# Kernel optimization log

Measured on AMD Instinct MI355X. Metric: run time of the kernel, lower is better.

Reference implementation:

```python
import jax, jax.numpy as jnp
import numpy as np
from jax import lax

EPS = 1e-7
N_CLASS = 10
ROUTINGS = 3
DIM_PRIMARY = 8
DIM_DIGIT = 16


def squash(s, axis=-1):
    sq = jnp.sum(jnp.square(s), axis=axis, keepdims=True)
    scale = sq / (1.0 + sq) / jnp.sqrt(sq + EPS)
    return scale * s


def setup_inputs() -> dict:
    key = jax.random.key(0)
    ks = jax.random.split(key, 6)
    B, H, W, C = 16, 100, 64, 1
    x = jax.random.normal(ks[0], (B, H, W, C), dtype=jnp.float32)
    # conv1: 9x9, 1 -> 256, stride 1, valid, relu
    conv1_w = jax.random.normal(ks[1], (9, 9, 1, 256), dtype=jnp.float32) * 0.05
    conv1_b = jnp.zeros((256,), dtype=jnp.float32)
    # PrimaryCap conv: 9x9, 256 -> 32*8=256, stride 2, valid, linear
    pc_w = jax.random.normal(ks[2], (9, 9, 256, 256), dtype=jnp.float32) * 0.02
    pc_b = jnp.zeros((256,), dtype=jnp.float32)
    # primary caps: conv1 out 92x56 -> pc conv out 42x24 -> 42*24*32 = 32256 caps
    n_in_caps = 42 * 24 * 32
    caps_W = jax.random.normal(ks[3], (N_CLASS, n_in_caps, DIM_DIGIT, DIM_PRIMARY), dtype=jnp.float32) * 0.05
    return {"x": x, "conv1_w": conv1_w, "conv1_b": conv1_b, "pc_w": pc_w, "pc_b": pc_b, "caps_W": caps_W}


def reference(x, conv1_w, conv1_b, pc_w, pc_b, caps_W):
    dn = ("NHWC", "HWIO", "NHWC")
    # Conv1 + relu: [B,92,56,256]
    y = lax.conv_general_dilated(x, conv1_w, (1, 1), "VALID", dimension_numbers=dn) + conv1_b
    y = jax.nn.relu(y)
    # PrimaryCap conv (stride 2): [B,42,24,256]
    p = lax.conv_general_dilated(y, pc_w, (2, 2), "VALID", dimension_numbers=dn) + pc_b
    B = p.shape[0]
    # reshape to capsules [B, I, 8] and squash
    u = squash(p.reshape(B, -1, DIM_PRIMARY))
    # predictions u_hat[b,j,i,d] = W[j,i,d,k] u[b,i,k]  -> [B, J, I, 16]
    u_hat = jnp.einsum("bik,jidk->bjid", u, caps_W)
    # dynamic routing
    b = jnp.zeros(u_hat.shape[:3], dtype=u_hat.dtype)  # [B, J, I]
    v = None
    for r in range(ROUTINGS):
        c = jax.nn.softmax(b, axis=1)  # over output capsules J
        s = jnp.einsum("bji,bjid->bjd", c, u_hat)
        v = squash(s)  # [B, J, 16]
        if r < ROUTINGS - 1:
            b = b + jnp.einsum("bjd,bjid->bji", v, u_hat)
    return v
```

## Files before the change

### kernel.cpp

```cpp
#include <hip/hip_runtime.h>
#include <hip/hip_bf16.h>
#include <hip/hip_fp16.h>
#include <stdint.h>

typedef __bf16 bf16x8_t __attribute__((ext_vector_type(8)));
typedef float  f32x4_t  __attribute__((ext_vector_type(4)));

#define PLANE_H   (16L * 32256 * 32)
#define PSTRIDE_H 4128768L

__device__ __forceinline__ void gld_lds16(const void* g, void* l) {
    __builtin_amdgcn_global_load_lds(
        (const __attribute__((address_space(1))) uint32_t*)g,
        (__attribute__((address_space(3))) uint32_t*)l, 16, 0, 0);
}

__global__ __launch_bounds__(256) void k_conv1(
    const float* __restrict__ x, const float* __restrict__ w,
    const float* __restrict__ bias, __hip_bfloat16* __restrict__ y)
{
    const int b  = blockIdx.x / 92;
    const int oh = blockIdx.x % 92;
    const int oc = threadIdx.x;
    float wr[81];
#pragma unroll
    for (int t = 0; t < 81; ++t) wr[t] = w[t * 256 + oc];
    const float bs = bias[oc];
    const float* xb = x + (b * 100 + oh) * 64;
    __hip_bfloat16* yb = y + ((b * 92 + oh) * 56) * 256 + oc;
    for (int owg = 0; owg < 56; owg += 4) {
        float a0 = bs, a1 = bs, a2 = bs, a3 = bs;
#pragma unroll
        for (int kh = 0; kh < 9; ++kh) {
            const float* xr = xb + kh * 64 + owg;
            float xv[12];
#pragma unroll
            for (int t = 0; t < 12; ++t) xv[t] = xr[t];
#pragma unroll
            for (int kw = 0; kw < 9; ++kw) {
                const float wv = wr[kh * 9 + kw];
                a0 = fmaf(xv[kw + 0], wv, a0);
                a1 = fmaf(xv[kw + 1], wv, a1);
                a2 = fmaf(xv[kw + 2], wv, a2);
                a3 = fmaf(xv[kw + 3], wv, a3);
            }
        }
        yb[(owg + 0) * 256] = __float2bfloat16(fmaxf(a0, 0.f));
        yb[(owg + 1) * 256] = __float2bfloat16(fmaxf(a1, 0.f));
        yb[(owg + 2) * 256] = __float2bfloat16(fmaxf(a2, 0.f));
        yb[(owg + 3) * 256] = __float2bfloat16(fmaxf(a3, 0.f));
    }
}

__global__ __launch_bounds__(256) void k_wt(
    const float* __restrict__ w, __hip_bfloat16* __restrict__ wt)
{
    const int idx = blockIdx.x * 256 + threadIdx.x;
    const int oc  = idx / 20736;
    const int k   = idx - oc * 20736;
    wt[idx] = __float2bfloat16(w[k * 256 + oc]);
}

__global__ __launch_bounds__(256, 4) void k_pcconv3(
    const __hip_bfloat16* __restrict__ y,
    const __hip_bfloat16* __restrict__ wt,
    __half* __restrict__ pbase)
{
    __shared__ __hip_bfloat16 lA[128 * 64];
    __shared__ __hip_bfloat16 lB[128 * 64];
    const int gx  = blockIdx.x;
    const int nb  = gx & 1;
    const int tm  = gx >> 1;
    const int mbx = (tm & 7) * 16 + (tm >> 3);
    if (mbx >= 126) return;
    const int z = blockIdx.y;
    __half* __restrict__ p = pbase + (long)z * PSTRIDE_H;

    const int tid  = threadIdx.x;
    const int lane = tid & 63;
    const int w    = tid >> 6;
    const int oct  = lane >> 3;
    const int c    = (lane & 7) ^ oct;

    int ybaseA[4], wbB[4];
#pragma unroll
    for (int j = 0; j < 4; ++j) {
        const int r  = w * 32 + j * 8 + oct;
        const int m  = mbx * 128 + r;
        const int b  = m / 1008;
        const int rm = m - b * 1008;
        const int oh = rm / 24;
        const int ow = rm - oh * 24;
        ybaseA[j] = ((b * 92 + 2 * oh) * 56 + 2 * ow) * 256 + c * 8;
        wbB[j]    = (nb * 128 + r) * 20736 + c * 8;
    }

    f32x4_t acc[4][4];
#pragma unroll
    for (int mi = 0; mi < 4; ++mi)
#pragma unroll
        for (int ni = 0; ni < 4; ++ni)
            acc[mi][ni] = (f32x4_t){0.f, 0.f, 0.f, 0.f};

    const int mw = (w >> 1) * 64;
    const int nw = (w & 1) * 64;
    const int lr = lane & 15;
    const int lq = lane >> 4;
    const int koff0 = ((lq + 0) ^ (lr & 7)) * 8;
    const int koff1 = ((lq + 4) ^ (lr & 7)) * 8;

    const int off = (gx * 11 + z * 5) % 27;
    for (int it = 0; it < 27; ++it) {
        const int kc   = z * 27 + ((it + off) % 27);
        const int k0   = kc * 64;
        const int khw  = k0 >> 8;
        const int ic0  = k0 & 255;
        const int kh   = khw / 9;
        const int kw2  = khw - kh * 9;
        const int aoff = (kh * 56 + kw2) * 256 + ic0;
        __syncthreads();
#pragma unroll
        for (int j = 0; j < 4; ++j)
            gld_lds16(y + ybaseA[j] + aoff, &lA[(w * 32 + j * 8) * 64 + lane * 8]);
#pragma unroll
        for (int j = 0; j < 4; ++j)
            gld_lds16(wt + wbB[j] + k0, &lB[(w * 32 + j * 8) * 64 + lane * 8]);
        __builtin_amdgcn_s_waitcnt(0);
        __syncthreads();
#pragma unroll
        for (int t = 0; t < 2; ++t) {
            const int koff = t ? koff1 : koff0;
            bf16x8_t af[4], bfr[4];
#pragma unroll
            for (int mi = 0; mi < 4; ++mi)
                af[mi] = *(const bf16x8_t*)&lA[(mw + mi * 16 + lr) * 64 + koff];
#pragma unroll
            for (int ni = 0; ni < 4; ++ni)
                bfr[ni] = *(const bf16x8_t*)&lB[(nw + ni * 16 + lr) * 64 + koff];
#pragma unroll
            for (int mi = 0; mi < 4; ++mi)
#pragma unroll
                for (int ni = 0; ni < 4; ++ni)
                    acc[mi][ni] = __builtin_amdgcn_mfma_f32_16x16x32_bf16(
                        af[mi], bfr[ni], acc[mi][ni], 0, 0, 0);
        }
    }
#pragma unroll
    for (int mi = 0; mi < 4; ++mi)
#pragma unroll
        for (int ni = 0; ni < 4; ++ni) {
            const int col = nb * 128 + nw + ni * 16 + lr;
#pragma unroll
            for (int rr = 0; rr < 4; ++rr) {
                const int row = mbx * 128 + mw + mi * 16 + lq * 4 + rr;
                p[(long)row * 256 + col] = __float2half(acc[mi][ni][rr]);
            }
        }
}

__global__ __launch_bounds__(512, 2) void k_pcconv8(
    const __hip_bfloat16* __restrict__ y,
    const __hip_bfloat16* __restrict__ wt,
    __half* __restrict__ pbase)
{
    extern __shared__ __hip_bfloat16 sm[];
    __hip_bfloat16* sA = sm;
    __hip_bfloat16* sB = sm + 32768;

    const int mblk = blockIdx.x;
    const int z    = blockIdx.y;
    __half* __restrict__ p = pbase + (long)z * PSTRIDE_H;

    const int tid  = threadIdx.x;
    const int lane = tid & 63;
    const int w    = tid >> 6;
    const int wm   = w >> 2;
    const int wn   = w & 3;
    const int oct  = lane >> 3;
    const int c    = (lane & 7) ^ oct;

    int ybs[4], wbs[4];
#pragma unroll
    for (int i64 = 0; i64 < 4; ++i64) {
        const int r  = i64 * 64 + w * 8 + oct;
        const int m  = mblk * 256 + r;
        const int b  = m / 1008;
        const int rm = m - b * 1008;
        const int oh = rm / 24;
        const int ow = rm - oh * 24;
        ybs[i64] = ((b * 92 + 2 * oh) * 56 + 2 * ow) * 256 + c * 8;
        wbs[i64] = r * 20736 + c * 8;
    }
    const int kbase = z * 1728;

    auto aoffk = [&](int k0) {
        const int khw = k0 >> 8;
        const int kh  = khw / 9;
        return (kh * 56 + (khw - kh * 9)) * 256 + (k0 & 255);
    };
    auto stA = [&](int i64, int buf, int aoff) {
        gld_lds16(y + ybs[i64] + aoff, sA + buf * 16384 + (i64 * 64 + w * 8) * 64 + lane * 8);
    };
    auto stB = [&](int i64, int buf, int k0) {
        gld_lds16(wt + wbs[i64] + k0, sB + buf * 16384 + (i64 * 64 + w * 8) * 64 + lane * 8);
    };

    f32x4_t acc[2][4][2][2];
#pragma unroll
    for (int mh = 0; mh < 2; ++mh)
#pragma unroll
        for (int mi = 0; mi < 4; ++mi)
#pragma unroll
            for (int nh = 0; nh < 2; ++nh)
#pragma unroll
                for (int ni = 0; ni < 2; ++ni)
                    acc[mh][mi][nh][ni] = (f32x4_t){0.f, 0.f, 0.f, 0.f};

    const int lr = lane & 15;
    const int lq = lane >> 4;
    const int koff0 = ((lq + 0) ^ (lr & 7)) * 8;
    const int koff1 = ((lq + 4) ^ (lr & 7)) * 8;

    bf16x8_t af[4][2], bf0[2][2], bf1[2][2];

#define RD_A(CUR, MH)                                                                   \
    _Pragma("unroll") for (int mi = 0; mi < 4; ++mi) {                                  \
        const __hip_bfloat16* ap =                                                      \
            sA + (CUR) * 16384 + (wm * 128 + (MH) * 64 + mi * 16 + lr) * 64;            \
        af[mi][0] = *(const bf16x8_t*)(ap + koff0);                                     \
        af[mi][1] = *(const bf16x8_t*)(ap + koff1);                                     \
    }
#define RD_B(DST, CUR, NH)                                                              \
    _Pragma("unroll") for (int ni = 0; ni < 2; ++ni) {                                  \
        const __hip_bfloat16* bp =                                                      \
            sB + (CUR) * 16384 + (wn * 64 + (NH) * 32 + ni * 16 + lr) * 64;             \
        DST[ni][0] = *(const bf16x8_t*)(bp + koff0);                                    \
        DST[ni][1] = *(const bf16x8_t*)(bp + koff1);                                    \
    }
#define MFMA_Q(MH, NH, BF)                                                              \
    _Pragma("unroll") for (int mi = 0; mi < 4; ++mi)                                    \
    _Pragma("unroll") for (int ni = 0; ni < 2; ++ni) {                                  \
        acc[MH][mi][NH][ni] = __builtin_amdgcn_mfma_f32_16x16x32_bf16(                  \
            af[mi][0], BF[ni][0], acc[MH][mi][NH][ni], 0, 0, 0);                        \
        acc[MH][mi][NH][ni] = __builtin_amdgcn_mfma_f32_16x16x32_bf16(                  \
            af[mi][1], BF[ni][1], acc[MH][mi][NH][ni], 0, 0, 0);                        \
    }

    {
        const int k0 = kbase;
        const int ao = aoffk(k0);
        stB(0, 0, k0); stB(1, 0, k0); stB(2, 0, k0); stB(3, 0, k0);
        stA(0, 0, ao); stA(2, 0, ao); stA(1, 0, ao); stA(3, 0, ao);
    }
    asm volatile("s_waitcnt vmcnt(2)" ::: "memory");
    __builtin_amdgcn_s_barrier();

    for (int kt = 0; kt < 26; ++kt) {
        const int cur = kt & 1, nxt = cur ^ 1;
        const int k0n = kbase + (kt + 1) * 64;
        const int aon = aoffk(k0n);
        RD_A(cur, 0);
        RD_B(bf0, cur, 0);
        RD_B(bf1, cur, 1);
        stB(0, nxt, k0n); stB(1, nxt, k0n); stB(2, nxt, k0n); stB(3, nxt, k0n);
        __builtin_amdgcn_s_barrier();
        asm volatile("s_waitcnt lgkmcnt(0)" ::: "memory");
        __builtin_amdgcn_s_setprio(1);
        MFMA_Q(0, 0, bf0);
        MFMA_Q(0, 1, bf1);
        __builtin_amdgcn_s_setprio(0);
        asm volatile("s_waitcnt vmcnt(4)" ::: "memory");
        __builtin_amdgcn_s_barrier();
        RD_A(cur, 1);
        stA(0, nxt, aon); stA(2, nxt, aon); stA(1, nxt, aon); stA(3, nxt, aon);
        __builtin_amdgcn_s_barrier();
        asm volatile("s_waitcnt lgkmcnt(0)" ::: "memory");
        __builtin_amdgcn_s_setprio(1);
        MFMA_Q(1, 1, bf1);
        MFMA_Q(1, 0, bf0);
        __builtin_amdgcn_s_setprio(0);
        asm volatile("s_waitcnt vmcnt(2)" ::: "memory");
        __builtin_amdgcn_s_barrier();
    }

    RD_A(0, 0);
    RD_B(bf0, 0, 0);
    RD_B(bf1, 0, 1);
    __builtin_amdgcn_s_barrier();
    asm volatile("s_waitcnt lgkmcnt(0)" ::: "memory");
    __builtin_amdgcn_s_setprio(1);
    MFMA_Q(0, 0, bf0);
    MFMA_Q(0, 1, bf1);
    __builtin_amdgcn_s_setprio(0);
    asm volatile("s_waitcnt vmcnt(0)" ::: "memory");
    __builtin_amdgcn_s_barrier();
    RD_A(0, 1);
    asm volatile("s_waitcnt lgkmcnt(0)" ::: "memory");
    __builtin_amdgcn_s_setprio(1);
    MFMA_Q(1, 1, bf1);
    MFMA_Q(1, 0, bf0);
    __builtin_amdgcn_s_setprio(0);

#undef RD_A
#undef RD_B
#undef MFMA_Q

#pragma unroll
    for (int mh = 0; mh < 2; ++mh)
#pragma unroll
        for (int mi = 0; mi < 4; ++mi)
#pragma unroll
            for (int nh = 0; nh < 2; ++nh)
#pragma unroll
                for (int ni = 0; ni < 2; ++ni) {
                    const int col = wn * 64 + nh * 32 + ni * 16 + lr;
#pragma unroll
                    for (int rr = 0; rr < 4; ++rr) {
                        const int row = mblk * 256 + wm * 128 + mh * 64 + mi * 16 + lq * 4 + rr;
                        p[(long)row * 256 + col] = __float2half(acc[mh][mi][nh][ni][rr]);
                    }
                }
}

__global__ __launch_bounds__(256) void k_squash(
    const __half* __restrict__ Ph, const float* __restrict__ bias, float* __restrict__ u)
{
    const int g = blockIdx.x * 256 + threadIdx.x;
    const long base = (long)g * 8;
    const int cb = (g & 31) * 8;
    float v[8];
#pragma unroll
    for (int t = 0; t < 8; ++t) v[t] = bias[cb + t];
#pragma unroll
    for (int z = 0; z < 12; ++z) {
        const uint4 r = *(const uint4*)(Ph + z * PSTRIDE_H + base);
        const unsigned wd[4] = {r.x, r.y, r.z, r.w};
#pragma unroll
        for (int h2 = 0; h2 < 4; ++h2) {
            const __half2 hh = *(const __half2*)&wd[h2];
            v[h2 * 2 + 0] += __low2float(hh);
            v[h2 * 2 + 1] += __high2float(hh);
        }
    }
    float sq = 0.f;
#pragma unroll
    for (int t = 0; t < 8; ++t) sq += v[t] * v[t];
    const float sc = sq / ((1.f + sq) * sqrtf(sq + 1e-7f));
#pragma unroll
    for (int t = 0; t < 8; ++t) u[base + t] = v[t] * sc;
}

__global__ __launch_bounds__(256) void k_uhat2(
    const float* __restrict__ u, const float* __restrict__ W, __half* __restrict__ uh,
    float* __restrict__ sp0)
{
    __shared__ __half lbuf[8 * 64 * 32];
    __shared__ float red[4 * 256];
    const int bh   = blockIdx.x;
    const int ic   = blockIdx.y;
    const int tid  = threadIdx.x;
    const int lane = tid & 63;
    const int wv   = tid >> 6;
    const int q    = tid & 3;
    const int il   = tid >> 2;
    const int i    = ic * 64 + il;

    for (int jg = 0; jg < 5; ++jg) {
        const float* wb0 = W + ((long)(2 * jg) * 32256 + i) * 128 + q * 32;
        const float* wb1 = wb0 + (long)32256 * 128;
        float4 w0[8], w1[8];
#pragma unroll
        for (int t = 0; t < 8; ++t) w0[t] = *(const float4*)(wb0 + t * 4);
#pragma unroll
        for (int t = 0; t < 8; ++t) w1[t] = *(const float4*)(wb1 + t * 4);
        if (jg) __syncthreads();
#pragma unroll
        for (int b = 0; b < 8; ++b) {
            const float* up = u + ((bh * 8 + b) * 32256 + i) * 8;
            const float4 u0 = *(const float4*)up;
            const float4 u1 = *(const float4*)(up + 4);
            union { __half h[8]; uint4 v; } pk;
#pragma unroll
            for (int d = 0; d < 4; ++d) {
                const float4 a = w0[2 * d], cc = w0[2 * d + 1];
                pk.h[d] = __float2half(
                    a.x * u0.x + a.y * u0.y + a.z * u0.z + a.w * u0.w +
                    cc.x * u1.x + cc.y * u1.y + cc.z * u1.z + cc.w * u1.w);
            }
#pragma unroll
            for (int d = 0; d < 4; ++d) {
                const float4 a = w1[2 * d], cc = w1[2 * d + 1];
                pk.h[4 + d] = __float2half(
                    a.x * u0.x + a.y * u0.y + a.z * u0.z + a.w * u0.w +
                    cc.x * u1.x + cc.y * u1.y + cc.z * u1.z + cc.w * u1.w);
            }
            *(uint4*)&lbuf[(b * 64 + il) * 32 + q * 8] = pk.v;
            float rv[8];
#pragma unroll
            for (int t = 0; t < 8; ++t) rv[t] = __half2float(pk.h[t]);
#pragma unroll
            for (int t = 0; t < 8; ++t) {
                rv[t] += __shfl_xor(rv[t], 4);
                rv[t] += __shfl_xor(rv[t], 8);
                rv[t] += __shfl_xor(rv[t], 16);
                rv[t] += __shfl_xor(rv[t], 32);
            }
            if (lane < 4) {
#pragma unroll
                for (int t = 0; t < 8; ++t)
                    red[wv * 256 + b * 32 + (t >> 2) * 16 + q * 4 + (t & 3)] = rv[t];
            }
        }
        __syncthreads();
        __half* pb = uh + (long)jg * PLANE_H + ((long)(bh * 8) * 32256 + ic * 64) * 32;
#pragma unroll
        for (int b = 0; b < 8; ++b) {
            const uint4 v = *(const uint4*)&lbuf[b * 2048 + tid * 8];
            *(uint4*)(pb + (long)b * (32256 * 32) + tid * 8) = v;
        }
        {
            const float v = red[tid] + red[256 + tid] + red[512 + tid] + red[768 + tid];
            const int bb = tid >> 5, j2 = (tid >> 4) & 1, dd = tid & 15;
            atomicAdd(&sp0[((bh * 8 + bb) * 10 + (2 * jg + j2)) * 16 + dd], 0.1f * v);
        }
    }
}

__global__ __launch_bounds__(256) void k_route4(
    const __half* __restrict__ uh, const float* __restrict__ vsum,
    float* __restrict__ sp)
{
    __shared__ float red[4 * 160];
    const int b     = blockIdx.x;
    const int chunk = blockIdx.y;
    const int tid   = threadIdx.x;
    const int lane  = tid & 63;
    const int wv    = tid >> 6;
    const int q     = lane & 3;
    const int ig    = lane >> 2;

    float vs[10][4];
#pragma unroll
    for (int j = 0; j < 10; ++j) {
        const float4 t = *(const float4*)(vsum + (b * 10 + j) * 16 + q * 4);
        vs[j][0] = t.x; vs[j][1] = t.y; vs[j][2] = t.z; vs[j][3] = t.w;
    }
    float acc[10][4];
#pragma unroll
    for (int j = 0; j < 10; ++j)
#pragma unroll
        for (int t = 0; t < 4; ++t) acc[j][t] = 0.f;

    const int ib = chunk * 576 + wv * 16 + ig;
    for (int ps = 0; ps < 9; ++ps) {
        const int i = ib + ps * 64;
        const long rb = ((long)b * 32256 + i) * 32 + q * 8;
        uint4 r[5];
#pragma unroll
        for (int jg = 0; jg < 5; ++jg)
            r[jg] = *(const uint4*)(uh + jg * PLANE_H + rb);
        float uhf[10][4];
#pragma unroll
        for (int jg = 0; jg < 5; ++jg) {
            const unsigned wd[4] = {r[jg].x, r[jg].y, r[jg].z, r[jg].w};
#pragma unroll
            for (int h2 = 0; h2 < 4; ++h2) {
                const __half2 hh = *(const __half2*)&wd[h2];
                const int j  = jg * 2 + (h2 >> 1);
                const int d0 = (h2 & 1) * 2;
                uhf[j][d0 + 0] = __low2float(hh);
                uhf[j][d0 + 1] = __high2float(hh);
            }
        }
        float logit[10];
#pragma unroll
        for (int j = 0; j < 10; ++j) {
            float lg = vs[j][0] * uhf[j][0] + vs[j][1] * uhf[j][1]
                     + vs[j][2] * uhf[j][2] + vs[j][3] * uhf[j][3];
            lg += __shfl_xor(lg, 1);
            lg += __shfl_xor(lg, 2);
            logit[j] = lg;
        }
        float mx = logit[0];
#pragma unroll
        for (int j = 1; j < 10; ++j) mx = fmaxf(mx, logit[j]);
        float den = 0.f, e[10];
#pragma unroll
        for (int j = 0; j < 10; ++j) { e[j] = __expf(logit[j] - mx); den += e[j]; }
        const float inv = __builtin_amdgcn_rcpf(den);
#pragma unroll
        for (int j = 0; j < 10; ++j) {
            const float c = e[j] * inv;
#pragma unroll
            for (int t = 0; t < 4; ++t) acc[j][t] = fmaf(c, uhf[j][t], acc[j][t]);
        }
    }
#pragma unroll
    for (int j = 0; j < 10; ++j)
#pragma unroll
        for (int t = 0; t < 4; ++t) {
            float v2 = acc[j][t];
            v2 += __shfl_xor(v2, 4);
            v2 += __shfl_xor(v2, 8);
            v2 += __shfl_xor(v2, 16);
            v2 += __shfl_xor(v2, 32);
            if (lane < 4) red[wv * 160 + j * 16 + q * 4 + t] = v2;
        }
    __syncthreads();
    if (tid < 160) {
        const float s = red[tid] + red[160 + tid] + red[320 + tid] + red[480 + tid];
        atomicAdd(&sp[b * 160 + tid], s);
    }
}

__global__ void k_finish(const float* __restrict__ sp, float* __restrict__ vsum,
                         float* __restrict__ out, const int fin)
{
    const int t = threadIdx.x;
    if (t >= 160) return;
    const float* s = sp + t * 16;
    float sv[16]; float sq = 0.f;
#pragma unroll
    for (int d = 0; d < 16; ++d) { sv[d] = s[d]; sq += sv[d] * sv[d]; }
    const float sc = sq / ((1.f + sq) * sqrtf(sq + 1e-7f));
    if (fin) {
#pragma unroll
        for (int d = 0; d < 16; ++d) out[t * 16 + d] = sv[d] * sc;
    } else {
        float* vp = vsum + t * 16;
#pragma unroll
        for (int d = 0; d < 16; ++d) vp[d] += sv[d] * sc;
    }
}

extern "C" void kernel_launch(void* const* d_in, const int* in_sizes, int n_in,
                              void* d_out, int out_size, void* d_ws, size_t ws_size,
                              hipStream_t stream)
{
    const float* x   = (const float*)d_in[0];
    const float* c1w = (const float*)d_in[1];
    const float* c1b = (const float*)d_in[2];
    const float* pcw = (const float*)d_in[3];
    const float* pcb = (const float*)d_in[4];
    const float* cW  = (const float*)d_in[5];
    float* out = (float*)d_out;

    char* ws = (char*)d_ws;
    float* u  = (float*)(ws);
    __half* Ph = (__half*)(ws + 16515072);
    __hip_bfloat16* y  = (__hip_bfloat16*)(ws + 115605504);
    __hip_bfloat16* wt = (__hip_bfloat16*)(ws + 157810688);
    __half* uh = (__half*)(ws + 16515072);
    float* sp   = (float*)(ws + 181665792);
    float* vsum = (float*)(ws + 181696512);

    static int pc8_ok = -1;
    if (pc8_ok < 0)
        pc8_ok = (hipFuncSetAttribute((const void*)k_pcconv8,
                    hipFuncAttributeMaxDynamicSharedMemorySize, 131072) == hipSuccess)
                 ? 1 : 0;

    hipMemsetAsync(sp, 0, (3 * 2560 + 2560) * 4, stream);

    k_conv1<<<16 * 92, 256, 0, stream>>>(x, c1w, c1b, y);
    k_wt<<<20736, 256, 0, stream>>>(pcw, wt);
    if (pc8_ok)
        k_pcconv8<<<dim3(63, 12), 512, 131072, stream>>>(y, wt, Ph);
    else
        k_pcconv3<<<dim3(256, 12), 256, 0, stream>>>(y, wt, Ph);
    k_squash<<<2016, 256, 0, stream>>>(Ph, pcb, u);
    k_uhat2<<<dim3(2, 504), 256, 0, stream>>>(u, cW, uh, sp);
    k_finish<<<1, 256, 0, stream>>>(sp, vsum, out, 0);
    k_route4<<<dim3(16, 56), 256, 0, stream>>>(uh, vsum, sp + 2560);
    k_finish<<<1, 256, 0, stream>>>(sp + 2560, vsum, out, 0);
    k_route4<<<dim3(16, 56), 256, 0, stream>>>(uh, vsum, sp + 5120);
    k_finish<<<1, 256, 0, stream>>>(sp + 5120, vsum, out, 1);
}
```

Measured before the change: 651.9 us.

## Remap pcconv blocks per XCD, reuse caps weights across batches, prefetch routing loads

Three changes. The primary-capsule conv remaps its block IDs so that consecutive logical tiles (12 z-slices of the same M block) land on the same XCD, which should improve L2 sharing of the A tile. The u_hat kernel now loops over both batch halves inside one block, so each caps_W slice is loaded once instead of twice, halving weight traffic at the cost of half as many blocks. The routing kernel software-pipelines its u_hat loads one iteration ahead, which uses more registers.

```diff
diff --git a/kernel.cpp b/kernel.cpp
--- a/kernel.cpp
+++ b/kernel.cpp
@@ -167,8 +167,12 @@
     __hip_bfloat16* sA = sm;
     __hip_bfloat16* sB = sm + 32768;
 
-    const int mblk = blockIdx.x;
-    const int z    = blockIdx.y;
+    const int pphys = blockIdx.y * 63 + blockIdx.x;
+    const int xcd   = pphys & 7;
+    const int slot  = pphys >> 3;
+    const int L     = (xcd < 4 ? xcd * 95 : 380 + (xcd - 4) * 94) + slot;
+    const int mblk  = L / 12;
+    const int z     = L - mblk * 12;
     __half* __restrict__ p = pbase + (long)z * PSTRIDE_H;
 
     const int tid  = threadIdx.x;
@@ -356,8 +360,7 @@
 {
     __shared__ __half lbuf[8 * 64 * 32];
     __shared__ float red[4 * 256];
-    const int bh   = blockIdx.x;
-    const int ic   = blockIdx.y;
+    const int ic   = blockIdx.x;
     const int tid  = threadIdx.x;
     const int lane = tid & 63;
     const int wv   = tid >> 6;
@@ -373,55 +376,57 @@
         for (int t = 0; t < 8; ++t) w0[t] = *(const float4*)(wb0 + t * 4);
 #pragma unroll
         for (int t = 0; t < 8; ++t) w1[t] = *(const float4*)(wb1 + t * 4);
-        if (jg) __syncthreads();
-#pragma unroll
-        for (int b = 0; b < 8; ++b) {
-            const float* up = u + ((bh * 8 + b) * 32256 + i) * 8;
-            const float4 u0 = *(const float4*)up;
-            const float4 u1 = *(const float4*)(up + 4);
-            union { __half h[8]; uint4 v; } pk;
-#pragma unroll
-            for (int d = 0; d < 4; ++d) {
-                const float4 a = w0[2 * d], cc = w0[2 * d + 1];
-                pk.h[d] = __float2half(
-                    a.x * u0.x + a.y * u0.y + a.z * u0.z + a.w * u0.w +
-                    cc.x * u1.x + cc.y * u1.y + cc.z * u1.z + cc.w * u1.w);
+        for (int bh = 0; bh < 2; ++bh) {
+            if (jg | bh) __syncthreads();
+#pragma unroll
+            for (int b = 0; b < 8; ++b) {
+                const float* up = u + ((bh * 8 + b) * 32256 + i) * 8;
+                const float4 u0 = *(const float4*)up;
+                const float4 u1 = *(const float4*)(up + 4);
+                union { __half h[8]; uint4 v; } pk;
+#pragma unroll
+                for (int d = 0; d < 4; ++d) {
+                    const float4 a = w0[2 * d], cc = w0[2 * d + 1];
+                    pk.h[d] = __float2half(
+                        a.x * u0.x + a.y * u0.y + a.z * u0.z + a.w * u0.w +
+                        cc.x * u1.x + cc.y * u1.y + cc.z * u1.z + cc.w * u1.w);
+                }
+#pragma unroll
+                for (int d = 0; d < 4; ++d) {
+                    const float4 a = w1[2 * d], cc = w1[2 * d + 1];
+                    pk.h[4 + d] = __float2half(
+                        a.x * u0.x + a.y * u0.y + a.z * u0.z + a.w * u0.w +
+                        cc.x * u1.x + cc.y * u1.y + cc.z * u1.z + cc.w * u1.w);
+                }
+                *(uint4*)&lbuf[(b * 64 + il) * 32 + q * 8] = pk.v;
+                float rv[8];
+#pragma unroll
+                for (int t = 0; t < 8; ++t) rv[t] = __half2float(pk.h[t]);
+#pragma unroll
+                for (int t = 0; t < 8; ++t) {
+                    rv[t] += __shfl_xor(rv[t], 4);
+                    rv[t] += __shfl_xor(rv[t], 8);
+                    rv[t] += __shfl_xor(rv[t], 16);
+                    rv[t] += __shfl_xor(rv[t], 32);
+                }
+                if (lane < 4) {
+#pragma unroll
+                    for (int t = 0; t < 8; ++t)
+                        red[wv * 256 + b * 32 + (t >> 2) * 16 + q * 4 + (t & 3)] = rv[t];
+                }
             }
-#pragma unroll
-            for (int d = 0; d < 4; ++d) {
-                const float4 a = w1[2 * d], cc = w1[2 * d + 1];
-                pk.h[4 + d] = __float2half(
-                    a.x * u0.x + a.y * u0.y + a.z * u0.z + a.w * u0.w +
-                    cc.x * u1.x + cc.y * u1.y + cc.z * u1.z + cc.w * u1.w);
+            __syncthreads();
+            __half* pb = uh + (long)jg * PLANE_H + ((long)(bh * 8) * 32256 + ic * 64) * 32;
+#pragma unroll
+            for (int b = 0; b < 8; ++b) {
+                const uint4 v = *(const uint4*)&lbuf[b * 2048 + tid * 8];
+                *(uint4*)(pb + (long)b * (32256 * 32) + tid * 8) = v;
             }
-            *(uint4*)&lbuf[(b * 64 + il) * 32 + q * 8] = pk.v;
-            float rv[8];
-#pragma unroll
-            for (int t = 0; t < 8; ++t) rv[t] = __half2float(pk.h[t]);
-#pragma unroll
-            for (int t = 0; t < 8; ++t) {
-                rv[t] += __shfl_xor(rv[t], 4);
-                rv[t] += __shfl_xor(rv[t], 8);
-                rv[t] += __shfl_xor(rv[t], 16);
-                rv[t] += __shfl_xor(rv[t], 32);
+            {
+                const float v = red[tid] + red[256 + tid] + red[512 + tid] + red[768 + tid];
+                const int bb = tid >> 5, j2 = (tid >> 4) & 1, dd = tid & 15;
+                atomicAdd(&sp0[((bh * 8 + bb) * 10 + (2 * jg + j2)) * 16 + dd], 0.1f * v);
             }
-            if (lane < 4) {
-#pragma unroll
-                for (int t = 0; t < 8; ++t)
-                    red[wv * 256 + b * 32 + (t >> 2) * 16 + q * 4 + (t & 3)] = rv[t];
-            }
-        }
-        __syncthreads();
-        __half* pb = uh + (long)jg * PLANE_H + ((long)(bh * 8) * 32256 + ic * 64) * 32;
-#pragma unroll
-        for (int b = 0; b < 8; ++b) {
-            const uint4 v = *(const uint4*)&lbuf[b * 2048 + tid * 8];
-            *(uint4*)(pb + (long)b * (32256 * 32) + tid * 8) = v;
-        }
-        {
-            const float v = red[tid] + red[256 + tid] + red[512 + tid] + red[768 + tid];
-            const int bb = tid >> 5, j2 = (tid >> 4) & 1, dd = tid & 15;
-            atomicAdd(&sp0[((bh * 8 + bb) * 10 + (2 * jg + j2)) * 16 + dd], 0.1f * v);
         }
     }
 }
@@ -452,13 +457,19 @@
         for (int t = 0; t < 4; ++t) acc[j][t] = 0.f;
 
     const int ib = chunk * 576 + wv * 16 + ig;
+    const long rbase = ((long)b * 32256 + ib) * 32 + q * 8;
+    uint4 r[5];
+#pragma unroll
+    for (int jg = 0; jg < 5; ++jg)
+        r[jg] = *(const uint4*)(uh + jg * PLANE_H + rbase);
     for (int ps = 0; ps < 9; ++ps) {
-        const int i = ib + ps * 64;
-        const long rb = ((long)b * 32256 + i) * 32 + q * 8;
-        uint4 r[5];
-#pragma unroll
-        for (int jg = 0; jg < 5; ++jg)
-            r[jg] = *(const uint4*)(uh + jg * PLANE_H + rb);
+        uint4 rn[5];
+        if (ps < 8) {
+            const long rb2 = rbase + (long)(ps + 1) * 2048;
+#pragma unroll
+            for (int jg = 0; jg < 5; ++jg)
+                rn[jg] = *(const uint4*)(uh + jg * PLANE_H + rb2);
+        }
         float uhf[10][4];
 #pragma unroll
         for (int jg = 0; jg < 5; ++jg) {
@@ -493,6 +504,10 @@
             const float c = e[j] * inv;
 #pragma unroll
             for (int t = 0; t < 4; ++t) acc[j][t] = fmaf(c, uhf[j][t], acc[j][t]);
+        }
+        if (ps < 8) {
+#pragma unroll
+            for (int jg = 0; jg < 5; ++jg) r[jg] = rn[jg];
         }
     }
 #pragma unroll
@@ -569,7 +584,7 @@
     else
         k_pcconv3<<<dim3(256, 12), 256, 0, stream>>>(y, wt, Ph);
     k_squash<<<2016, 256, 0, stream>>>(Ph, pcb, u);
-    k_uhat2<<<dim3(2, 504), 256, 0, stream>>>(u, cW, uh, sp);
+    k_uhat2<<<504, 256, 0, stream>>>(u, cW, uh, sp);
     k_finish<<<1, 256, 0, stream>>>(sp, vsum, out, 0);
     k_route4<<<dim3(16, 56), 256, 0, stream>>>(uh, vsum, sp + 2560);
     k_finish<<<1, 256, 0, stream>>>(sp + 2560, vsum, out, 0);
```

After: 662.6 us. About the same (+1.6%).
